# Kernel optimization log

Measured on AMD Instinct MI355X. Metric: run time of the kernel, lower is better.

The kernel has to match this reference:

```python
import jax, jax.numpy as jnp
import numpy as np

B, S, D, H, DFF = 4, 2048, 1024, 16, 4096
DK = D // H
EPS = 1e-6


def setup_inputs() -> dict:
    key = jax.random.key(0)
    ks = jax.random.split(key, 8)
    s = 0.02
    return {
        "x": jax.random.normal(ks[0], (B, S, D), jnp.float32),
        "src_mask": jnp.ones((B, 1, 1, S), jnp.int32),
        "w_q": jax.random.normal(ks[1], (D, D), jnp.float32) * s,
        "w_k": jax.random.normal(ks[2], (D, D), jnp.float32) * s,
        "w_v": jax.random.normal(ks[3], (D, D), jnp.float32) * s,
        "w_o": jax.random.normal(ks[4], (D, D), jnp.float32) * s,
        "w1": jax.random.normal(ks[5], (DFF, D), jnp.float32) * s,
        "b1": jnp.zeros((DFF,), jnp.float32),
        "w2": jax.random.normal(ks[6], (D, DFF), jnp.float32) * s,
        "b2": jnp.zeros((D,), jnp.float32),
        "gamma1": jnp.ones((1,), jnp.float32),
        "beta1": jnp.zeros((1,), jnp.float32),
        "gamma2": jnp.ones((1,), jnp.float32),
        "beta2": jnp.zeros((1,), jnp.float32),
    }


def layernorm(x, gamma, beta):
    # matches torch source: unbiased std (ddof=1), eps added to std, scalar gamma/beta
    mean = jnp.mean(x, axis=-1, keepdims=True)
    std = jnp.std(x, axis=-1, keepdims=True, ddof=1)
    return gamma * (x - mean) / (std + EPS) + beta


def mha(x, w_q, w_k, w_v, w_o):
    # Linear(bias=False): y = x @ W.T
    q = (x @ w_q.T).reshape(B, S, H, DK).transpose(0, 2, 1, 3)  # [B,H,S,DK]
    k = (x @ w_k.T).reshape(B, S, H, DK).transpose(0, 2, 1, 3)
    v = (x @ w_v.T).reshape(B, S, H, DK).transpose(0, 2, 1, 3)
    scores = jnp.einsum('bhqd,bhkd->bhqk', q, k) / np.float32(np.sqrt(DK))
    # NOTE: source calls attention.masked_fill(...) without assigning the result,
    # so the mask has no effect; faithfully replicated (mask unused).
    attn = jax.nn.softmax(scores, axis=-1)
    ctx = jnp.einsum('bhqk,bhkd->bhqd', attn, v)  # [B,H,S,DK]
    ctx = ctx.transpose(0, 2, 1, 3).reshape(B, S, D)
    return ctx @ w_o.T


def ffn(x, w1, b1, w2, b2):
    return jax.nn.relu(x @ w1.T + b1) @ w2.T + b2


def reference(x, src_mask, w_q, w_k, w_v, w_o, w1, b1, w2, b2,
              gamma1, beta1, gamma2, beta2):
    # pre-norm residual blocks; dropout is identity in eval
    x = x + mha(layernorm(x, gamma1, beta1), w_q, w_k, w_v, w_o)
    x = x + ffn(layernorm(x, gamma2, beta2), w1, b1, w2, b2)
    return x
```

## Files before the change

kernel.cpp:

```cpp
#include <hip/hip_runtime.h>
#include <hip/hip_bf16.h>

#define DEV static __device__ __forceinline__

typedef unsigned short u16;
typedef float fp32x4 __attribute__((ext_vector_type(4)));
typedef short bf16x8 __attribute__((ext_vector_type(8)));
typedef short bf16x4 __attribute__((ext_vector_type(4)));

DEV float bf2f(u16 u) { return __uint_as_float(((unsigned)u) << 16); }
DEV u16 f2bf(float f) {
  unsigned x = __float_as_uint(f);
  x += 0x7fffu + ((x >> 16) & 1u);
  return (u16)(x >> 16);
}

DEV unsigned cvt_pk_bf16(float a, float b) {
  unsigned r;
  asm("v_cvt_pk_bf16_f32 %0, %1, %2" : "=v"(r) : "v"(a), "v"(b));
  return r;
}

DEV void gload_lds16(const void* g, void* l) {
  __builtin_amdgcn_global_load_lds(
      (__attribute__((address_space(1))) void*)(unsigned long long)g,
      (__attribute__((address_space(3))) void*)(unsigned int)(unsigned long long)l,
      16, 0, 0);
}

__global__ __launch_bounds__(256) void cvt_kernel(const float* __restrict__ in,
                                                  u16* __restrict__ out) {
  const int i = blockIdx.x * 256 + threadIdx.x;
  const fp32x4 v = ((const fp32x4*)in)[i];
  bf16x4 o;
#pragma unroll
  for (int j = 0; j < 4; j++) o[j] = (short)f2bf(v[j]);
  ((bf16x4*)out)[i] = o;
}

__global__ __launch_bounds__(256) void ln_kernel(const float* __restrict__ x,
                                                 u16* __restrict__ y,
                                                 const float* __restrict__ gamma,
                                                 const float* __restrict__ beta) {
  const int row = blockIdx.x;
  const int t = threadIdx.x;
  const fp32x4 v = ((const fp32x4*)(x + (size_t)row * 1024))[t];
  float s = v[0] + v[1] + v[2] + v[3];
  float ss = v[0] * v[0] + v[1] * v[1] + v[2] * v[2] + v[3] * v[3];
#pragma unroll
  for (int o = 32; o > 0; o >>= 1) {
    s += __shfl_down(s, o);
    ss += __shfl_down(ss, o);
  }
  __shared__ float rs[4], rss[4];
  const int w = t >> 6;
  if ((t & 63) == 0) { rs[w] = s; rss[w] = ss; }
  __syncthreads();
  const float S = rs[0] + rs[1] + rs[2] + rs[3];
  const float SS = rss[0] + rss[1] + rss[2] + rss[3];
  const float mean = S * (1.0f / 1024.0f);
  const float var = fmaxf((SS - 1024.0f * mean * mean) * (1.0f / 1023.0f), 0.0f);
  const float sc = gamma[0] / (sqrtf(var) + 1e-6f);
  const float be = beta[0];
  bf16x4 o;
#pragma unroll
  for (int j = 0; j < 4; j++) o[j] = (short)f2bf((v[j] - mean) * sc + be);
  ((bf16x4*)(y + (size_t)row * 1024))[t] = o;
}

template <int EPI>
__global__ __launch_bounds__(256, 2) void gemm_bt(
    const u16* __restrict__ A, const u16* __restrict__ W, u16* __restrict__ Cb,
    float* __restrict__ Cf, const float* __restrict__ bias,
    const float* __restrict__ resid, int M, int N, int K) {
  __shared__ u16 sA[128 * 32];
  __shared__ u16 sB[128 * 32];
  const int t = threadIdx.x;
  const int lane = t & 63;
  const int w = t >> 6;
  const int wr = (w >> 1) * 64;
  const int wc = (w & 1) * 64;
  const int lr = lane & 15;
  const int hi = lane >> 4;

  const int nwgx = gridDim.x;
  const int orig = blockIdx.y * nwgx + blockIdx.x;
  const int cpx = (nwgx * gridDim.y) >> 3;
  const int logical = (orig & 7) * cpx + (orig >> 3);
  const int bx = logical % nwgx, by = logical / nwgx;

  const u16* gA = A + (size_t)(by * 128 + (t >> 2)) * K + (t & 3) * 8;
  const u16* gB = W + (size_t)(bx * 128 + (t >> 2)) * K + (t & 3) * 8;
  const size_t rstep = (size_t)64 * K;
  u16* lA = &sA[t * 8];
  u16* lB = &sB[t * 8];

  const fp32x4 zero4 = {0.f, 0.f, 0.f, 0.f};
  fp32x4 acc[4][4];
#pragma unroll
  for (int i = 0; i < 4; i++)
#pragma unroll
    for (int j = 0; j < 4; j++) acc[i][j] = zero4;

  for (int k0 = 0; k0 < K; k0 += 32) {
    gload_lds16(gA, lA);
    gload_lds16(gA + rstep, lA + 2048);
    gload_lds16(gB, lB);
    gload_lds16(gB + rstep, lB + 2048);
    gA += 32;
    gB += 32;
    __syncthreads();
    bf16x8 af[4], bfr[4];
#pragma unroll
    for (int i = 0; i < 4; i++)
      af[i] = *(const bf16x8*)&sA[(wr + i * 16 + lr) * 32 + hi * 8];
#pragma unroll
    for (int j = 0; j < 4; j++)
      bfr[j] = *(const bf16x8*)&sB[(wc + j * 16 + lr) * 32 + hi * 8];
#pragma unroll
    for (int i = 0; i < 4; i++)
#pragma unroll
      for (int j = 0; j < 4; j++)
        acc[i][j] =
            __builtin_amdgcn_mfma_f32_16x16x32_bf16(af[i], bfr[j], acc[i][j], 0, 0, 0);
    __syncthreads();
  }

  const int row0 = by * 128 + wr + hi * 4;
  const int col0 = bx * 128 + wc + lr;
  float bj[4] = {0.f, 0.f, 0.f, 0.f};
  if (EPI == 1 || EPI == 3) {
#pragma unroll
    for (int j = 0; j < 4; j++) bj[j] = bias[col0 + j * 16];
  }
#pragma unroll
  for (int i = 0; i < 4; i++) {
#pragma unroll
    for (int r = 0; r < 4; r++) {
      const size_t row = (size_t)(row0 + i * 16 + r);
#pragma unroll
      for (int j = 0; j < 4; j++) {
        const int col = col0 + j * 16;
        float v = acc[i][j][r];
        if (EPI == 1) v = fmaxf(v + bj[j], 0.f);
        if (EPI == 3) v += bj[j];
        if (EPI >= 2) {
          v += resid[row * N + col];
          Cf[row * N + col] = v;
        } else {
          Cb[row * N + col] = f2bf(v);
        }
      }
    }
  }
}

__global__ __launch_bounds__(256) void vtrans_kernel(const u16* __restrict__ V,
                                                     u16* __restrict__ VT) {
  const int st = blockIdx.x;
  const int h = blockIdx.y;
  const int b = blockIdx.z;
  const int t = threadIdx.x;
  const int r = t >> 2, c0 = (t & 3) * 16;
  __shared__ u16 sT[64][72];

  const u16* src = V + ((size_t)(b * 2048 + st * 64 + r)) * 1024 + h * 64 + c0;
  bf16x8 v0 = *(const bf16x8*)src;
  bf16x8 v1 = *(const bf16x8*)(src + 8);
  const int cb = c0 ^ ((r >> 4) << 4);
  *(bf16x8*)&sT[r][cb] = v0;
  *(bf16x8*)&sT[r][cb + 8] = v1;
  __syncthreads();

  const int dc = r ^ ((c0 >> 4) << 4);
  bf16x8 o0, o1;
#pragma unroll
  for (int i = 0; i < 8; i++) o0[i] = sT[c0 + i][dc];
#pragma unroll
  for (int i = 0; i < 8; i++) o1[i] = sT[c0 + 8 + i][dc];
  u16* dst = VT + ((size_t)((b * 16 + h) * 64 + r)) * 2048 + st * 64 + c0;
  *(bf16x8*)dst = o0;
  *(bf16x8*)(dst + 8) = o1;
}

__global__ __launch_bounds__(256, 2) void attn_kernel(const u16* __restrict__ Q,
                                                      const u16* __restrict__ K,
                                                      const u16* __restrict__ VT,
                                                      u16* __restrict__ O) {
  const int orig = blockIdx.x + 32 * (blockIdx.y + 16 * blockIdx.z);
  const int logical = (orig & 7) * 256 + (orig >> 3);
  const int qt = logical & 31;
  const int h = (logical >> 5) & 15;
  const int b = logical >> 9;

  const int t = threadIdx.x, lane = t & 63, w = t >> 6;
  const int lr = lane & 15, hi = lane >> 4;

  __shared__ u16 sK[64][72];
  __shared__ u16 sVT[64][72];
  __shared__ u16 sQP[64][72];

  const size_t base = ((size_t)b * 2048) * 1024 + (size_t)h * 64;
  const size_t vbase = (((size_t)b * 16 + h) * 64) * 2048;
  const int r = t >> 2, c0 = (t & 3) * 16;

  {
    const float qs = 0.125f * 1.44269504f;
    const u16* src = Q + base + (size_t)(qt * 64 + r) * 1024 + c0;
    bf16x8 u0 = *(const bf16x8*)src;
    bf16x8 u1 = *(const bf16x8*)(src + 8);
    union { unsigned u[4]; bf16x8 v; } q0, q1;
#pragma unroll
    for (int j = 0; j < 4; j++)
      q0.u[j] = cvt_pk_bf16(bf2f((u16)u0[2 * j]) * qs, bf2f((u16)u0[2 * j + 1]) * qs);
#pragma unroll
    for (int j = 0; j < 4; j++)
      q1.u[j] = cvt_pk_bf16(bf2f((u16)u1[2 * j]) * qs, bf2f((u16)u1[2 * j + 1]) * qs);
    *(bf16x8*)&sQP[r][c0] = q0.v;
    *(bf16x8*)&sQP[r][c0 + 8] = q1.v;
  }
  __syncthreads();
  const int qrow = w * 16 + lr;
  bf16x8 qreg0 = *(const bf16x8*)&sQP[qrow][hi * 8];
  bf16x8 qreg1 = *(const bf16x8*)&sQP[qrow][32 + hi * 8];

  bf16x8 kA, kB, vA, vB;
  {
    const u16* ks = K + base + (size_t)r * 1024 + c0;
    kA = *(const bf16x8*)ks;
    kB = *(const bf16x8*)(ks + 8);
    const u16* vs = VT + vbase + (size_t)r * 2048 + c0;
    vA = *(const bf16x8*)vs;
    vB = *(const bf16x8*)(vs + 8);
  }

  const fp32x4 zero4 = {0.f, 0.f, 0.f, 0.f};
  fp32x4 onT[4];
#pragma unroll
  for (int df = 0; df < 4; df++) onT[df] = zero4;
  float mrun = -1e30f, lrun = 0.f;

  for (int kt = 0; kt < 32; ++kt) {
    __syncthreads();
    *(bf16x8*)&sK[r][c0] = kA;
    *(bf16x8*)&sK[r][c0 + 8] = kB;
    *(bf16x8*)&sVT[r][c0] = vA;
    *(bf16x8*)&sVT[r][c0 + 8] = vB;
    __syncthreads();
    if (kt < 31) {
      const u16* kn = K + base + (size_t)((kt + 1) * 64 + r) * 1024 + c0;
      kA = *(const bf16x8*)kn;
      kB = *(const bf16x8*)(kn + 8);
      const u16* vn = VT + vbase + (size_t)r * 2048 + (kt + 1) * 64 + c0;
      vA = *(const bf16x8*)vn;
      vB = *(const bf16x8*)(vn + 8);
    }

    fp32x4 sc[4];
    __builtin_amdgcn_s_setprio(1);
#pragma unroll
    for (int kk = 0; kk < 4; kk++) {
      fp32x4 a = zero4;
      bf16x8 kf0 = *(const bf16x8*)&sK[kk * 16 + lr][hi * 8];
      bf16x8 kf1 = *(const bf16x8*)&sK[kk * 16 + lr][32 + hi * 8];
      a = __builtin_amdgcn_mfma_f32_16x16x32_bf16(kf0, qreg0, a, 0, 0, 0);
      a = __builtin_amdgcn_mfma_f32_16x16x32_bf16(kf1, qreg1, a, 0, 0, 0);
      sc[kk] = a;
    }
    __builtin_amdgcn_s_setprio(0);

    float mloc = -1e30f;
#pragma unroll
    for (int kk = 0; kk < 4; kk++)
#pragma unroll
      for (int rr = 0; rr < 4; rr++) mloc = fmaxf(mloc, sc[kk][rr]);
    mloc = fmaxf(mloc, __shfl_xor(mloc, 16));
    mloc = fmaxf(mloc, __shfl_xor(mloc, 32));
    const float mnew = fmaxf(mrun, mloc);
    const float alpha = exp2f(mrun - mnew);
    float psum = 0.f;
#pragma unroll
    for (int kk = 0; kk < 4; kk++) {
      float p0 = exp2f(sc[kk][0] - mnew), p1 = exp2f(sc[kk][1] - mnew);
      float p2 = exp2f(sc[kk][2] - mnew), p3 = exp2f(sc[kk][3] - mnew);
      psum += (p0 + p1) + (p2 + p3);
      uint2 pk = {cvt_pk_bf16(p0, p1), cvt_pk_bf16(p2, p3)};
      *(uint2*)&sQP[qrow][kk * 16 + hi * 4] = pk;
    }
    psum += __shfl_xor(psum, 16);
    psum += __shfl_xor(psum, 32);
    lrun = lrun * alpha + psum;
    mrun = mnew;
#pragma unroll
    for (int df = 0; df < 4; df++) onT[df] *= alpha;

    __builtin_amdgcn_s_setprio(1);
#pragma unroll
    for (int df = 0; df < 4; df++) {
#pragma unroll
      for (int ks = 0; ks < 2; ks++) {
        bf16x8 vf = *(const bf16x8*)&sVT[df * 16 + lr][ks * 32 + hi * 8];
        bf16x8 pf = *(const bf16x8*)&sQP[qrow][ks * 32 + hi * 8];
        onT[df] = __builtin_amdgcn_mfma_f32_16x16x32_bf16(vf, pf, onT[df], 0, 0, 0);
      }
    }
    __builtin_amdgcn_s_setprio(0);
  }

  const float invl = 1.0f / lrun;
  u16* dst = O + base + (size_t)(qt * 64 + qrow) * 1024;
#pragma unroll
  for (int df = 0; df < 4; df++) {
    uint2 o2 = {cvt_pk_bf16(onT[df][0] * invl, onT[df][1] * invl),
                cvt_pk_bf16(onT[df][2] * invl, onT[df][3] * invl)};
    *(uint2*)&dst[df * 16 + hi * 4] = o2;
  }
}

extern "C" void kernel_launch(void* const* d_in, const int* in_sizes, int n_in,
                              void* d_out, int out_size, void* d_ws, size_t ws_size,
                              hipStream_t stream) {
  const float* x = (const float*)d_in[0];
  const float* wq = (const float*)d_in[2];
  const float* wk = (const float*)d_in[3];
  const float* wv = (const float*)d_in[4];
  const float* wo = (const float*)d_in[5];
  const float* w1 = (const float*)d_in[6];
  const float* b1 = (const float*)d_in[7];
  const float* w2 = (const float*)d_in[8];
  const float* b2 = (const float*)d_in[9];
  const float* g1 = (const float*)d_in[10];
  const float* be1 = (const float*)d_in[11];
  const float* g2 = (const float*)d_in[12];
  const float* be2 = (const float*)d_in[13];
  float* out = (float*)d_out;

  const size_t MB = 1024ull * 1024ull;
  char* ws = (char*)d_ws;
  if (ws_size < 136 * MB) return;

  u16* wqb = (u16*)(ws + 0 * MB);
  u16* wkb = (u16*)(ws + 2 * MB);
  u16* wvb = (u16*)(ws + 4 * MB);
  u16* wob = (u16*)(ws + 6 * MB);
  u16* w1b = (u16*)(ws + 8 * MB);
  u16* w2b = (u16*)(ws + 16 * MB);
  u16* Qb = (u16*)(ws + 24 * MB);
  u16* Kb = (u16*)(ws + 40 * MB);
  u16* Vb = (u16*)(ws + 56 * MB);
  u16* Ctx = (u16*)(ws + 72 * MB);
  u16* Hb = (u16*)(ws + 24 * MB);
  u16* Yb = (u16*)(ws + 88 * MB);
  u16* VTb = (u16*)(ws + 88 * MB);
  float* X2 = (float*)(ws + 104 * MB);

  dim3 blk(256);

  cvt_kernel<<<1024, blk, 0, stream>>>(wq, wqb);
  cvt_kernel<<<1024, blk, 0, stream>>>(wk, wkb);
  cvt_kernel<<<1024, blk, 0, stream>>>(wv, wvb);
  cvt_kernel<<<1024, blk, 0, stream>>>(wo, wob);
  cvt_kernel<<<4096, blk, 0, stream>>>(w1, w1b);
  cvt_kernel<<<4096, blk, 0, stream>>>(w2, w2b);

  ln_kernel<<<8192, blk, 0, stream>>>(x, Yb, g1, be1);

  gemm_bt<0><<<dim3(8, 64), blk, 0, stream>>>(Yb, wqb, Qb, nullptr, nullptr, nullptr,
                                              8192, 1024, 1024);
  gemm_bt<0><<<dim3(8, 64), blk, 0, stream>>>(Yb, wkb, Kb, nullptr, nullptr, nullptr,
                                              8192, 1024, 1024);
  gemm_bt<0><<<dim3(8, 64), blk, 0, stream>>>(Yb, wvb, Vb, nullptr, nullptr, nullptr,
                                              8192, 1024, 1024);
  vtrans_kernel<<<dim3(32, 16, 4), blk, 0, stream>>>(Vb, VTb);

  attn_kernel<<<dim3(32, 16, 4), blk, 0, stream>>>(Qb, Kb, VTb, Ctx);

  gemm_bt<2><<<dim3(8, 64), blk, 0, stream>>>(Ctx, wob, nullptr, X2, nullptr, x, 8192,
                                              1024, 1024);

  ln_kernel<<<8192, blk, 0, stream>>>(X2, Yb, g2, be2);

  gemm_bt<1><<<dim3(32, 64), blk, 0, stream>>>(Yb, w1b, Hb, nullptr, b1, nullptr, 8192,
                                               4096, 1024);

  gemm_bt<3><<<dim3(8, 64), blk, 0, stream>>>(Hb, w2b, nullptr, out, b2, X2, 8192, 1024,
                                              4096);
}
```

Measured before the change: 475.5 us.

## Fuse QKV projections into one GEMM, read V from global, lazy softmax rescale

Merges the three Q/K/V projection GEMMs into a single N=3072 GEMM whose epilogue routes each column block to the Q, K or V buffer, relying on the contiguous bf16 weight layout in the workspace. In attention, V^T fragments now come straight from global memory into registers instead of through LDS, and the separate sVT buffer is removed. The online softmax skips rescaling unless the running max grows by more than a threshold, which saves exp and multiply work per tile. The costs are more global-load latency exposed in the inner loop and exponent values bounded by about 2^11 before they are packed to bf16.

```diff
diff --git a/kernel.cpp b/kernel.cpp
--- a/kernel.cpp
+++ b/kernel.cpp
@@ -72,7 +72,8 @@
 __global__ __launch_bounds__(256, 2) void gemm_bt(
     const u16* __restrict__ A, const u16* __restrict__ W, u16* __restrict__ Cb,
     float* __restrict__ Cf, const float* __restrict__ bias,
-    const float* __restrict__ resid, int M, int N, int K) {
+    const float* __restrict__ resid, int M, int N, int K,
+    u16* __restrict__ CbK, u16* __restrict__ CbV) {
   __shared__ u16 sA[128 * 32];
   __shared__ u16 sB[128 * 32];
   const int t = threadIdx.x;
@@ -133,6 +134,13 @@
 #pragma unroll
     for (int j = 0; j < 4; j++) bj[j] = bias[col0 + j * 16];
   }
+  u16* qkvDst = nullptr;
+  int colL0 = 0;
+  if (EPI == 4) {
+    const int sel = col0 >> 10;
+    qkvDst = (sel == 0) ? Cb : (sel == 1 ? CbK : CbV);
+    colL0 = col0 & 1023;
+  }
 #pragma unroll
   for (int i = 0; i < 4; i++) {
 #pragma unroll
@@ -140,8 +148,12 @@
       const size_t row = (size_t)(row0 + i * 16 + r);
 #pragma unroll
       for (int j = 0; j < 4; j++) {
+        float v = acc[i][j][r];
+        if (EPI == 4) {
+          qkvDst[row * 1024 + colL0 + j * 16] = f2bf(v);
+          continue;
+        }
         const int col = col0 + j * 16;
-        float v = acc[i][j][r];
         if (EPI == 1) v = fmaxf(v + bj[j], 0.f);
         if (EPI == 3) v += bj[j];
         if (EPI >= 2) {
@@ -197,7 +209,6 @@
   const int lr = lane & 15, hi = lane >> 4;
 
   __shared__ u16 sK[64][72];
-  __shared__ u16 sVT[64][72];
   __shared__ u16 sQP[64][72];
 
   const size_t base = ((size_t)b * 2048) * 1024 + (size_t)h * 64;
@@ -224,14 +235,13 @@
   bf16x8 qreg0 = *(const bf16x8*)&sQP[qrow][hi * 8];
   bf16x8 qreg1 = *(const bf16x8*)&sQP[qrow][32 + hi * 8];
 
-  bf16x8 kA, kB, vA, vB;
+  const u16* vrow0 = VT + vbase + (size_t)lr * 2048 + hi * 8;
+
+  bf16x8 kA, kB;
   {
     const u16* ks = K + base + (size_t)r * 1024 + c0;
     kA = *(const bf16x8*)ks;
     kB = *(const bf16x8*)(ks + 8);
-    const u16* vs = VT + vbase + (size_t)r * 2048 + c0;
-    vA = *(const bf16x8*)vs;
-    vB = *(const bf16x8*)(vs + 8);
   }
 
   const fp32x4 zero4 = {0.f, 0.f, 0.f, 0.f};
@@ -244,17 +254,19 @@
     __syncthreads();
     *(bf16x8*)&sK[r][c0] = kA;
     *(bf16x8*)&sK[r][c0 + 8] = kB;
-    *(bf16x8*)&sVT[r][c0] = vA;
-    *(bf16x8*)&sVT[r][c0 + 8] = vB;
     __syncthreads();
     if (kt < 31) {
       const u16* kn = K + base + (size_t)((kt + 1) * 64 + r) * 1024 + c0;
       kA = *(const bf16x8*)kn;
       kB = *(const bf16x8*)(kn + 8);
-      const u16* vn = VT + vbase + (size_t)r * 2048 + (kt + 1) * 64 + c0;
-      vA = *(const bf16x8*)vn;
-      vB = *(const bf16x8*)(vn + 8);
-    }
+    }
+    bf16x8 vf[4][2];
+#pragma unroll
+    for (int df = 0; df < 4; df++)
+#pragma unroll
+      for (int ks = 0; ks < 2; ks++)
+        vf[df][ks] =
+            *(const bf16x8*)(vrow0 + (size_t)df * 16 * 2048 + kt * 64 + ks * 32);
 
     fp32x4 sc[4];
     __builtin_amdgcn_s_setprio(1);
@@ -269,39 +281,41 @@
     }
     __builtin_amdgcn_s_setprio(0);
 
-    float mloc = -1e30f;
-#pragma unroll
-    for (int kk = 0; kk < 4; kk++)
-#pragma unroll
-      for (int rr = 0; rr < 4; rr++) mloc = fmaxf(mloc, sc[kk][rr]);
+    float m0 = fmaxf(fmaxf(sc[0][0], sc[0][1]), fmaxf(sc[0][2], sc[0][3]));
+    float m1 = fmaxf(fmaxf(sc[1][0], sc[1][1]), fmaxf(sc[1][2], sc[1][3]));
+    float m2 = fmaxf(fmaxf(sc[2][0], sc[2][1]), fmaxf(sc[2][2], sc[2][3]));
+    float m3 = fmaxf(fmaxf(sc[3][0], sc[3][1]), fmaxf(sc[3][2], sc[3][3]));
+    float mloc = fmaxf(fmaxf(m0, m1), fmaxf(m2, m3));
     mloc = fmaxf(mloc, __shfl_xor(mloc, 16));
     mloc = fmaxf(mloc, __shfl_xor(mloc, 32));
-    const float mnew = fmaxf(mrun, mloc);
-    const float alpha = exp2f(mrun - mnew);
+    if (!__all(mloc - mrun <= 11.0f)) {
+      const float mnew = fmaxf(mrun, mloc);
+      const float alpha = exp2f(mrun - mnew);
+      lrun *= alpha;
+#pragma unroll
+      for (int df = 0; df < 4; df++) onT[df] *= alpha;
+      mrun = mnew;
+    }
     float psum = 0.f;
 #pragma unroll
     for (int kk = 0; kk < 4; kk++) {
-      float p0 = exp2f(sc[kk][0] - mnew), p1 = exp2f(sc[kk][1] - mnew);
-      float p2 = exp2f(sc[kk][2] - mnew), p3 = exp2f(sc[kk][3] - mnew);
+      float p0 = exp2f(sc[kk][0] - mrun), p1 = exp2f(sc[kk][1] - mrun);
+      float p2 = exp2f(sc[kk][2] - mrun), p3 = exp2f(sc[kk][3] - mrun);
       psum += (p0 + p1) + (p2 + p3);
       uint2 pk = {cvt_pk_bf16(p0, p1), cvt_pk_bf16(p2, p3)};
       *(uint2*)&sQP[qrow][kk * 16 + hi * 4] = pk;
     }
     psum += __shfl_xor(psum, 16);
     psum += __shfl_xor(psum, 32);
-    lrun = lrun * alpha + psum;
-    mrun = mnew;
-#pragma unroll
-    for (int df = 0; df < 4; df++) onT[df] *= alpha;
+    lrun += psum;
 
     __builtin_amdgcn_s_setprio(1);
 #pragma unroll
     for (int df = 0; df < 4; df++) {
 #pragma unroll
       for (int ks = 0; ks < 2; ks++) {
-        bf16x8 vf = *(const bf16x8*)&sVT[df * 16 + lr][ks * 32 + hi * 8];
         bf16x8 pf = *(const bf16x8*)&sQP[qrow][ks * 32 + hi * 8];
-        onT[df] = __builtin_amdgcn_mfma_f32_16x16x32_bf16(vf, pf, onT[df], 0, 0, 0);
+        onT[df] = __builtin_amdgcn_mfma_f32_16x16x32_bf16(vf[df][ks], pf, onT[df], 0, 0, 0);
       }
     }
     __builtin_amdgcn_s_setprio(0);
@@ -339,6 +353,7 @@
   char* ws = (char*)d_ws;
   if (ws_size < 136 * MB) return;
 
+  u16* wqkv = (u16*)(ws + 0 * MB);
   u16* wqb = (u16*)(ws + 0 * MB);
   u16* wkb = (u16*)(ws + 2 * MB);
   u16* wvb = (u16*)(ws + 4 * MB);
@@ -365,24 +380,20 @@
 
   ln_kernel<<<8192, blk, 0, stream>>>(x, Yb, g1, be1);
 
-  gemm_bt<0><<<dim3(8, 64), blk, 0, stream>>>(Yb, wqb, Qb, nullptr, nullptr, nullptr,
-                                              8192, 1024, 1024);
-  gemm_bt<0><<<dim3(8, 64), blk, 0, stream>>>(Yb, wkb, Kb, nullptr, nullptr, nullptr,
-                                              8192, 1024, 1024);
-  gemm_bt<0><<<dim3(8, 64), blk, 0, stream>>>(Yb, wvb, Vb, nullptr, nullptr, nullptr,
-                                              8192, 1024, 1024);
+  gemm_bt<4><<<dim3(24, 64), blk, 0, stream>>>(Yb, wqkv, Qb, nullptr, nullptr, nullptr,
+                                               8192, 3072, 1024, Kb, Vb);
   vtrans_kernel<<<dim3(32, 16, 4), blk, 0, stream>>>(Vb, VTb);
 
   attn_kernel<<<dim3(32, 16, 4), blk, 0, stream>>>(Qb, Kb, VTb, Ctx);
 
   gemm_bt<2><<<dim3(8, 64), blk, 0, stream>>>(Ctx, wob, nullptr, X2, nullptr, x, 8192,
-                                              1024, 1024);
+                                              1024, 1024, nullptr, nullptr);
 
   ln_kernel<<<8192, blk, 0, stream>>>(X2, Yb, g2, be2);
 
   gemm_bt<1><<<dim3(32, 64), blk, 0, stream>>>(Yb, w1b, Hb, nullptr, b1, nullptr, 8192,
-                                               4096, 1024);
+                                               4096, 1024, nullptr, nullptr);
 
   gemm_bt<3><<<dim3(8, 64), blk, 0, stream>>>(Hb, w2b, nullptr, out, b2, X2, 8192, 1024,
-                                              4096);
-}
+                                              4096, nullptr, nullptr);
+}
```

New measurement: 564.8 us. +18.8%, slower.
